# Performance work log

Hardware: AMD Instinct MI355X
Metric: run time of the kernel (lower is better)

The kernel has to match this reference:

```python
import jax, jax.numpy as jnp
import numpy as np

N, E, K, G = 50000, 800000, 3, 64
F_IN, F_HID, F_OUT, N_CLS = 128, 192, 128, 10
LAMBDA_MAX = 2.0  # PyG ChebConv default when lambda_max is None and normalization='sym'


def setup_inputs() -> dict:
    key = jax.random.key(0)
    ks = jax.random.split(key, 12)
    x = jax.random.normal(ks[0], (N, F_IN), dtype=jnp.float32)
    edge_index = jax.random.randint(ks[1], (2, E), 0, N)
    batch = jnp.sort(jax.random.randint(ks[2], (N,), 0, G))

    def mkW(k, fi, fo):
        return jax.random.normal(k, (K, fi, fo), dtype=jnp.float32) / np.float32(np.sqrt(K * fi))

    W1 = mkW(ks[3], F_IN, F_HID)
    b1 = jax.random.normal(ks[4], (F_HID,), dtype=jnp.float32) * 0.01
    W2 = mkW(ks[5], F_HID, F_HID)
    b2 = jax.random.normal(ks[6], (F_HID,), dtype=jnp.float32) * 0.01
    W3 = mkW(ks[7], F_HID, F_OUT)
    b3 = jax.random.normal(ks[8], (F_OUT,), dtype=jnp.float32) * 0.01
    fc_w = jax.random.normal(ks[9], (F_OUT, N_CLS), dtype=jnp.float32) / np.float32(np.sqrt(F_OUT))
    fc_b = jax.random.normal(ks[10], (N_CLS,), dtype=jnp.float32) * 0.01
    return {"x": x, "edge_index": edge_index, "batch": batch,
            "W1": W1, "b1": b1, "W2": W2, "b2": b2, "W3": W3, "b3": b3,
            "fc_w": fc_w, "fc_b": fc_b}


def reference(x, edge_index, batch, W1, b1, W2, b2, W3, b3, fc_w, fc_b):
    row, col = edge_index[0], edge_index[1]
    # symmetric scaled Laplacian: L_hat = (2/lmax) * (I - D^-1/2 A D^-1/2) - I
    deg = jax.ops.segment_sum(jnp.ones((E,), x.dtype), row, num_segments=N)
    dis = jnp.where(deg > 0, jax.lax.rsqrt(jnp.maximum(deg, 1e-12)), 0.0)
    scale = 2.0 / LAMBDA_MAX
    w_edge = (-scale) * dis[row] * dis[col]  # off-diagonal entries of L_hat
    diag_w = scale - 1.0                      # diagonal entries (0 when lmax=2)

    def prop(h):  # h: [N, F] -> L_hat @ h
        return jax.ops.segment_sum(w_edge[:, None] * h[col], row, num_segments=N) + diag_w * h

    def cheb_conv(h, W, b):
        Tx0 = h
        out = Tx0 @ W[0]
        Tx1 = prop(Tx0)
        out = out + Tx1 @ W[1]
        for k in range(2, K):
            Tx2 = 2.0 * prop(Tx1) - Tx0
            out = out + Tx2 @ W[k]
            Tx0, Tx1 = Tx1, Tx2
        return out + b

    h = cheb_conv(x, W1, b1)
    h = cheb_conv(h, W2, b2)
    h = cheb_conv(h, W3, b3)

    # global mean pool over graphs
    sums = jax.ops.segment_sum(h, batch, num_segments=G)
    cnts = jax.ops.segment_sum(jnp.ones((N,), h.dtype), batch, num_segments=G)
    pooled = sums / jnp.maximum(cnts, 1.0)[:, None]  # [G, F_OUT]

    logits = pooled @ fc_w + fc_b
    return jax.nn.log_softmax(logits, axis=1)
```

## Files before the change

### kernel.cpp

```cpp
#include <hip/hip_runtime.h>
#include <math.h>

#define N_NODES 50000
#define N_EDGES 800000
#define N_GRAPHS 64
#define F_INN 128
#define F_HID 192
#define F_OUTT 128
#define N_CLS 10

typedef short short8 __attribute__((ext_vector_type(8)));
typedef float f32x4 __attribute__((ext_vector_type(4)));

static __device__ inline unsigned short f2bf(float f) {
    unsigned int u = __float_as_uint(f);
    unsigned int r = (u + 0x7FFFu + ((u >> 16) & 1u)) >> 16;
    return (unsigned short)r;
}
static __device__ inline float bf2f(unsigned short h) {
    return __uint_as_float(((unsigned int)h) << 16);
}

__global__ void k_deg(const int* __restrict__ row, int* __restrict__ cnt,
                      int* __restrict__ rank) {
    int e = blockIdx.x * 256 + threadIdx.x;
    if (e < N_EDGES) rank[e] = atomicAdd(&cnt[row[e]], 1);
}

__global__ void k_scan1(const int* __restrict__ cnt, int* __restrict__ rp,
                        int* __restrict__ part, float* __restrict__ dis) {
    __shared__ int s[256];
    int base = blockIdx.x * 512;
    int i0 = base + 2 * threadIdx.x;
    int v0 = (i0 < N_NODES) ? cnt[i0] : 0;
    int v1 = (i0 + 1 < N_NODES) ? cnt[i0 + 1] : 0;
    if (i0 < N_NODES) dis[i0] = v0 > 0 ? rsqrtf((float)v0) : 0.f;
    if (i0 + 1 < N_NODES) dis[i0 + 1] = v1 > 0 ? rsqrtf((float)v1) : 0.f;
    int tsum = v0 + v1;
    s[threadIdx.x] = tsum;
    __syncthreads();
    for (int off = 1; off < 256; off <<= 1) {
        int val = (threadIdx.x >= off) ? s[threadIdx.x - off] : 0;
        __syncthreads();
        s[threadIdx.x] += val;
        __syncthreads();
    }
    int excl = s[threadIdx.x] - tsum;
    if (i0 < N_NODES) rp[i0] = excl;
    if (i0 + 1 < N_NODES) rp[i0 + 1] = excl + v0;
    if (threadIdx.x == 255) part[blockIdx.x] = s[255];
}

__global__ void k_scan3(int* __restrict__ rp, const int* __restrict__ part,
                        int nb) {
    __shared__ int s[128];
    int t = threadIdx.x;
    int b = blockIdx.x;
    if (t < 128) s[t] = (t < b && t < nb) ? part[t] : 0;
    __syncthreads();
    for (int off = 64; off > 0; off >>= 1) {
        if (t < off) s[t] += s[t + off];
        __syncthreads();
    }
    int add = s[0];
    int i0 = b * 512 + 2 * t;
    if (i0 < N_NODES) rp[i0] += add;
    if (i0 + 1 < N_NODES) rp[i0 + 1] += add;
    if (b == 0 && t == 0) rp[N_NODES] = N_EDGES;
}

__global__ void k_scatter(const int* __restrict__ row, const int* __restrict__ col,
                          const float* __restrict__ dis, const int* __restrict__ rp,
                          const int* __restrict__ rank, int2* __restrict__ cw) {
    int e = blockIdx.x * 256 + threadIdx.x;
    if (e < N_EDGES) {
        int r = row[e], c = col[e];
        int pos = rp[r] + rank[e];
        int2 v;
        v.x = c;
        v.y = __float_as_int(-dis[r] * dis[c]);
        cw[pos] = v;
    }
}

#define NX (N_NODES * F_INN)
#define NW1 (3 * 128 * 192)
#define NW2 (3 * 192 * 192)
#define NW3 (3 * 192 * 128)
#define NPS (3 * N_GRAPHS * F_HID)
__global__ void k_convAll(const float* __restrict__ x, const float* __restrict__ W1,
                          const float* __restrict__ W2, const float* __restrict__ W3,
                          unsigned short* __restrict__ xb,
                          unsigned short* __restrict__ Wt1,
                          unsigned short* __restrict__ Wt2,
                          unsigned short* __restrict__ Wt3,
                          int* __restrict__ cnt, float* __restrict__ psum) {
    int idx = blockIdx.x * 256 + threadIdx.x;
    if (idx < NX) {
        xb[idx] = f2bf(x[idx]);
        return;
    }
    idx -= NX;
    if (idx < NW1) {
        int per = 128 * 192;
        int j = idx / per, r = idx - j * per;
        int k = r / 192, n = r - k * 192;
        float v = (j == 0) ? (W1[idx] - W1[idx + 2 * per])
                           : (j == 2 ? 2.f * W1[idx] : W1[idx]);
        Wt1[j * per + n * 128 + k] = f2bf(v);
        return;
    }
    idx -= NW1;
    if (idx < NW2) {
        int per = 192 * 192;
        int j = idx / per, r = idx - j * per;
        int k = r / 192, n = r - k * 192;
        float v = (j == 0) ? (W2[idx] - W2[idx + 2 * per])
                           : (j == 2 ? 2.f * W2[idx] : W2[idx]);
        Wt2[j * per + n * 192 + k] = f2bf(v);
        return;
    }
    idx -= NW2;
    if (idx < NW3) {
        int per = 192 * 128;
        int j = idx / per, r = idx - j * per;
        int k = r / 128, n = r - k * 128;
        float v = (j == 0) ? (W3[idx] - W3[idx + 2 * per])
                           : (j == 2 ? 2.f * W3[idx] : W3[idx]);
        Wt3[j * per + n * 192 + k] = f2bf(v);
        return;
    }
    idx -= NW3;
    if (idx < N_NODES) {
        cnt[idx] = 0;
        return;
    }
    idx -= N_NODES;
    if (idx < NPS) psum[idx] = 0.f;
}

template <int F, int POOL>
__global__ void k_spmv(const int* __restrict__ rp, const int2* __restrict__ cw,
                       const unsigned short* __restrict__ h,
                       unsigned short* __restrict__ y,
                       const int* __restrict__ batch, float* __restrict__ psum) {
    constexpr bool EX = (F > 128);
    constexpr int FU = F / 2;
    __shared__ float ps[POOL ? 192 : 1];
    __shared__ int gs[4];
    int wave = threadIdx.x >> 6;
    int lane = threadIdx.x & 63;
    int r = blockIdx.x * 4 + wave;
    int e0 = __builtin_amdgcn_readfirstlane(rp[r]);
    int e1 = __builtin_amdgcn_readfirstlane(rp[r + 1]);
    const unsigned int* hu = (const unsigned int*)h;
    float a0 = 0.f, a1 = 0.f, a2 = 0.f;
    int e = e0;
    for (; e + 8 <= e1; e += 8) {
        int colv[8];
        float wv[8];
#pragma unroll
        for (int u = 0; u < 8; u++) {
            int2 p = cw[e + u];
            colv[u] = __builtin_amdgcn_readfirstlane(p.x);
            wv[u] = __uint_as_float(__builtin_amdgcn_readfirstlane(p.y));
        }
        unsigned int g[8];
        unsigned short s[8];
#pragma unroll
        for (int u = 0; u < 8; u++) {
            g[u] = hu[colv[u] * FU + lane];
            if constexpr (EX) s[u] = h[colv[u] * F + 128 + lane];
        }
#pragma unroll
        for (int u = 0; u < 8; u++) {
            a0 += wv[u] * bf2f((unsigned short)g[u]);
            a1 += wv[u] * bf2f((unsigned short)(g[u] >> 16));
            if constexpr (EX) a2 += wv[u] * bf2f(s[u]);
        }
    }
    for (; e + 4 <= e1; e += 4) {
        int colv[4];
        float wv[4];
#pragma unroll
        for (int u = 0; u < 4; u++) {
            int2 p = cw[e + u];
            colv[u] = __builtin_amdgcn_readfirstlane(p.x);
            wv[u] = __uint_as_float(__builtin_amdgcn_readfirstlane(p.y));
        }
        unsigned int g[4];
        unsigned short s[4];
#pragma unroll
        for (int u = 0; u < 4; u++) {
            g[u] = hu[colv[u] * FU + lane];
            if constexpr (EX) s[u] = h[colv[u] * F + 128 + lane];
        }
#pragma unroll
        for (int u = 0; u < 4; u++) {
            a0 += wv[u] * bf2f((unsigned short)g[u]);
            a1 += wv[u] * bf2f((unsigned short)(g[u] >> 16));
            if constexpr (EX) a2 += wv[u] * bf2f(s[u]);
        }
    }
    for (; e < e1; e++) {
        int2 p = cw[e];
        int c = __builtin_amdgcn_readfirstlane(p.x);
        float w = __uint_as_float(__builtin_amdgcn_readfirstlane(p.y));
        unsigned int g = hu[c * FU + lane];
        a0 += w * bf2f((unsigned short)g);
        a1 += w * bf2f((unsigned short)(g >> 16));
        if constexpr (EX) a2 += w * bf2f(h[c * F + 128 + lane]);
    }
    if constexpr (POOL != 1) {
        ((unsigned int*)y)[r * FU + lane] =
            (unsigned int)f2bf(a0) | ((unsigned int)f2bf(a1) << 16);
        if constexpr (EX) y[r * F + 128 + lane] = f2bf(a2);
    }
    if constexpr (POOL != 0) {
        int t = threadIdx.x;
        if (t < 4) gs[t] = batch[blockIdx.x * 4 + t];
        if (t >= 64) ps[t - 64] = 0.f;
        __syncthreads();
        int g0 = gs[0], g3 = gs[3];
        if (g0 == g3) {
            atomicAdd(&ps[2 * lane], a0);
            atomicAdd(&ps[2 * lane + 1], a1);
            atomicAdd(&ps[128 + lane], a2);
            __syncthreads();
            if (wave == 0) {
                atomicAdd(&psum[g0 * 192 + 2 * lane], ps[2 * lane]);
                atomicAdd(&psum[g0 * 192 + 2 * lane + 1], ps[2 * lane + 1]);
                atomicAdd(&psum[g0 * 192 + 128 + lane], ps[128 + lane]);
            }
        } else {
            int gg = gs[wave];
            atomicAdd(&psum[gg * 192 + 2 * lane], a0);
            atomicAdd(&psum[gg * 192 + 2 * lane + 1], a1);
            atomicAdd(&psum[gg * 192 + 128 + lane], a2);
        }
    }
}

template <int Fin, int Fout, bool POOL>
__global__ __launch_bounds__(256) void k_gemm3(
    const unsigned short* __restrict__ A0, const unsigned short* __restrict__ A1,
    const unsigned short* __restrict__ A2, const unsigned short* __restrict__ Wt,
    const float* __restrict__ bias, unsigned short* __restrict__ C,
    const int* __restrict__ batch, float* __restrict__ psum) {
    constexpr int NF = Fout / 16;
    constexpr int BP = Fout / 64;
    __shared__ unsigned short As[128 * 40];
    __shared__ unsigned short Bs[Fout * 40];
    int t = threadIdx.x;
    int w = t >> 6;
    int lane = t & 63;
    int ml = lane & 15;
    int quad = lane >> 4;
    int mBase = blockIdx.x * 128;
    constexpr int per = Fin * Fout;

    f32x4 acc[2][NF];
#pragma unroll
    for (int i = 0; i < 2; i++)
#pragma unroll
        for (int jn = 0; jn < NF; jn++) acc[i][jn] = (f32x4){0.f, 0.f, 0.f, 0.f};

    int srow = t >> 2;
    int schunk = t & 3;
    constexpr int nChunks = (3 * Fin) >> 5;

    for (int ch = 0; ch < nChunks; ch++) {
        int kg = ch << 5;
        int j = kg / Fin;
        int kk = kg - j * Fin;
        const unsigned short* Aj = (j == 0) ? A0 : (j == 1) ? A1 : A2;
        if (ch > 0) __syncthreads();
#pragma unroll
        for (int pass = 0; pass < 2; pass++) {
            int row = srow + pass * 64;
            int gm = mBase + row;
            uint4 v = {0u, 0u, 0u, 0u};
            if (gm < N_NODES)
                v = *(const uint4*)(Aj + (size_t)gm * Fin + kk + schunk * 8);
            *(uint4*)&As[row * 40 + schunk * 8] = v;
        }
#pragma unroll
        for (int pass = 0; pass < BP; pass++) {
            int row = srow + pass * 64;
            const unsigned short* src =
                Wt + (size_t)j * per + (size_t)row * Fin + kk + schunk * 8;
            *(uint4*)&Bs[row * 40 + schunk * 8] = *(const uint4*)src;
        }
        __syncthreads();

        short8 afr[2];
#pragma unroll
        for (int i = 0; i < 2; i++)
            afr[i] = *(const short8*)&As[(w * 32 + i * 16 + ml) * 40 + quad * 8];
#pragma unroll
        for (int jn = 0; jn < NF; jn++) {
            short8 bfr = *(const short8*)&Bs[(jn * 16 + ml) * 40 + quad * 8];
#pragma unroll
            for (int i = 0; i < 2; i++)
                acc[i][jn] = __builtin_amdgcn_mfma_f32_16x16x32_bf16(
                    afr[i], bfr, acc[i][jn], 0, 0, 0);
        }
    }

    float biasv[NF];
#pragma unroll
    for (int jn = 0; jn < NF; jn++) biasv[jn] = bias[jn * 16 + ml];

#pragma unroll
    for (int i = 0; i < 2; i++) {
#pragma unroll
        for (int r = 0; r < 4; r++) {
            int m = mBase + w * 32 + i * 16 + quad * 4 + r;
            if (m < N_NODES) {
                unsigned short* cp = C + (size_t)m * Fout + ml;
#pragma unroll
                for (int jn = 0; jn < NF; jn++)
                    cp[jn * 16] = f2bf(acc[i][jn][r] + biasv[jn]);
            }
        }
    }
    if constexpr (POOL) {
        int m0 = mBase + w * 32;
        if (m0 >= N_NODES) return;
        int mlast = m0 + 31;
        if (mlast >= N_NODES) mlast = N_NODES - 1;
        int g0 = batch[m0];
        int g1 = batch[mlast];
        if (g0 == g1) {
#pragma unroll
            for (int jn = 0; jn < NF; jn++) {
                float pv = 0.f;
#pragma unroll
                for (int i = 0; i < 2; i++)
#pragma unroll
                    for (int r = 0; r < 4; r++) {
                        int m = m0 + i * 16 + quad * 4 + r;
                        if (m < N_NODES) pv += acc[i][jn][r] + biasv[jn];
                    }
                pv += __shfl_xor(pv, 16);
                pv += __shfl_xor(pv, 32);
                if (lane < 16) atomicAdd(&psum[g0 * Fout + ml + jn * 16], pv);
            }
        } else {
#pragma unroll
            for (int i = 0; i < 2; i++)
#pragma unroll
                for (int r = 0; r < 4; r++) {
                    int m = m0 + i * 16 + quad * 4 + r;
                    if (m < N_NODES) {
                        int g = batch[m];
#pragma unroll
                        for (int jn = 0; jn < NF; jn++)
                            atomicAdd(&psum[g * Fout + ml + jn * 16],
                                      acc[i][jn][r] + biasv[jn]);
                    }
                }
        }
    }
}

__global__ __launch_bounds__(128) void k_head2(
    const float* __restrict__ psum,
    const unsigned short* __restrict__ Wt3, const float* __restrict__ b3,
    const int* __restrict__ batch, const float* __restrict__ fcw,
    const float* __restrict__ fcb, float* __restrict__ out) {
    int g = blockIdx.x;
    int t = threadIdx.x;
    __shared__ float ps[3 * 192];
    __shared__ float m3[F_OUTT];
    __shared__ float sl[N_CLS];
    for (int i = t; i < 192; i += 128) {
        ps[i] = psum[g * 192 + i];
        ps[192 + i] = psum[N_GRAPHS * 192 + g * 192 + i];
        ps[384 + i] = psum[2 * N_GRAPHS * 192 + g * 192 + i];
    }
    __syncthreads();
    int a = 0, b = N_NODES;
    while (a < b) { int m = (a + b) >> 1; if (batch[m] < g) a = m + 1; else b = m; }
    int lo = a;
    a = lo; b = N_NODES;
    while (a < b) { int m = (a + b) >> 1; if (batch[m] < g + 1) a = m + 1; else b = m; }
    float inv = 1.f / fmaxf((float)(a - lo), 1.f);
    constexpr int per = 192 * F_OUTT;
    float accv = 0.f;
    const unsigned short* wp = Wt3 + (size_t)t * 192;
#pragma unroll 4
    for (int k = 0; k < 192; k += 8) {
        short8 v0 = *(const short8*)(wp + k);
        short8 v1 = *(const short8*)(wp + per + k);
        short8 v2 = *(const short8*)(wp + 2 * per + k);
#pragma unroll
        for (int j = 0; j < 8; j++)
            accv += ps[k + j] * bf2f((unsigned short)v0[j]) +
                    ps[192 + k + j] * bf2f((unsigned short)v1[j]) +
                    ps[384 + k + j] * bf2f((unsigned short)v2[j]);
    }
    m3[t] = accv * inv + b3[t];
    __syncthreads();
    if (t < N_CLS) {
        float l = fcb[t];
        for (int n = 0; n < F_OUTT; n++) l += m3[n] * fcw[n * N_CLS + t];
        sl[t] = l;
    }
    __syncthreads();
    if (t < N_CLS) {
        float mx = -1e30f;
        for (int i = 0; i < N_CLS; i++) mx = fmaxf(mx, sl[i]);
        float s = 0.f;
        for (int i = 0; i < N_CLS; i++) s += expf(sl[i] - mx);
        out[g * N_CLS + t] = sl[t] - mx - logf(s);
    }
}

extern "C" void kernel_launch(void* const* d_in, const int* in_sizes, int n_in,
                              void* d_out, int out_size, void* d_ws, size_t ws_size,
                              hipStream_t stream) {
    const float* x = (const float*)d_in[0];
    const int* ei = (const int*)d_in[1];
    const int* batch = (const int*)d_in[2];
    const float* W1 = (const float*)d_in[3];
    const float* b1 = (const float*)d_in[4];
    const float* W2 = (const float*)d_in[5];
    const float* b2 = (const float*)d_in[6];
    const float* W3 = (const float*)d_in[7];
    const float* b3 = (const float*)d_in[8];
    const float* fcw = (const float*)d_in[9];
    const float* fcb = (const float*)d_in[10];
    float* out = (float*)d_out;
    const int* row = ei;
    const int* col = ei + N_EDGES;

    char* p = (char*)d_ws;
    auto carve = [&](size_t bytes) {
        char* q = p;
        p += (bytes + 255) & ~(size_t)255;
        return q;
    };
    int* cnt = (int*)carve(N_NODES * 4);
    int* rank = (int*)carve((size_t)N_EDGES * 4);
    float* dis = (float*)carve(N_NODES * 4);
    int* rp = (int*)carve((N_NODES + 1) * 4);
    int* part = (int*)carve(128 * 4);
    int2* cw = (int2*)carve((size_t)N_EDGES * 8);
    unsigned short* xb = (unsigned short*)carve((size_t)N_NODES * F_INN * 2);
    size_t hbytes = (size_t)N_NODES * 192 * 2;
    unsigned short* bufA = (unsigned short*)carve(hbytes);
    unsigned short* bufB = (unsigned short*)carve(hbytes);
    unsigned short* bufC = (unsigned short*)carve(hbytes);
    unsigned short* bufD = (unsigned short*)carve(hbytes);
    unsigned short* Wt1 = (unsigned short*)carve(NW1 * 2);
    unsigned short* Wt2 = (unsigned short*)carve(NW2 * 2);
    unsigned short* Wt3 = (unsigned short*)carve(NW3 * 2);
    float* psum = (float*)carve(NPS * 4);
    float* psumX = psum;
    float* psumG1 = psum + N_GRAPHS * 192;
    float* psumG2 = psum + 2 * N_GRAPHS * 192;

    {
        int tot = NX + NW1 + NW2 + NW3 + N_NODES + NPS;
        k_convAll<<<(tot + 255) / 256, 256, 0, stream>>>(x, W1, W2, W3, xb, Wt1, Wt2,
                                                         Wt3, cnt, psum);
    }

    k_deg<<<(N_EDGES + 255) / 256, 256, 0, stream>>>(row, cnt, rank);
    int nb = (N_NODES + 511) / 512;
    k_scan1<<<nb, 256, 0, stream>>>(cnt, rp, part, dis);
    k_scan3<<<nb, 256, 0, stream>>>(rp, part, nb);
    k_scatter<<<(N_EDGES + 255) / 256, 256, 0, stream>>>(row, col, dis, rp, rank, cw);

    const int spmvGrid = N_NODES / 4;
    const int gemmGrid = (N_NODES + 127) / 128;

    k_spmv<128, 0><<<spmvGrid, 256, 0, stream>>>(rp, cw, xb, bufB, nullptr, nullptr);
    k_spmv<128, 0><<<spmvGrid, 256, 0, stream>>>(rp, cw, bufB, bufC, nullptr, nullptr);
    k_gemm3<128, 192, false><<<gemmGrid, 256, 0, stream>>>(xb, bufB, bufC, Wt1, b1,
                                                           bufA, batch, nullptr);
    k_spmv<192, 0><<<spmvGrid, 256, 0, stream>>>(rp, cw, bufA, bufB, nullptr, nullptr);
    k_spmv<192, 0><<<spmvGrid, 256, 0, stream>>>(rp, cw, bufB, bufC, nullptr, nullptr);
    k_gemm3<192, 192, true><<<gemmGrid, 256, 0, stream>>>(bufA, bufB, bufC, Wt2, b2,
                                                          bufD, batch, psumX);
    k_spmv<192, 2><<<spmvGrid, 256, 0, stream>>>(rp, cw, bufD, bufB, batch, psumG1);
    k_spmv<192, 1><<<spmvGrid, 256, 0, stream>>>(rp, cw, bufB, nullptr, batch, psumG2);

    k_head2<<<N_GRAPHS, 128, 0, stream>>>(psum, Wt3, b3, batch, fcw, fcb, out);
}
```

Before: 545.1 us.

## Move graph pooling out of SpMV and GEMM epilogues into dedicated pool kernel

Removes the fused mean-pool atomics from the layer-2 GEMM epilogue and the last two SpMV launches, so those kernels only write their outputs. The final SpMV now materializes its result to memory, and a new k_pool3 kernel reads the three layer-2 feature buffers and reduces them per graph with run-length accumulation before atomic adds. This cuts the per-block shared-memory atomics and syncthreads in SpMV, and the many global atomics. In exchange it adds an extra write plus a full re-read of three N×192 bf16 buffers and one more launch.

```diff
diff --git a/kernel.cpp b/kernel.cpp
--- a/kernel.cpp
+++ b/kernel.cpp
@@ -139,18 +139,16 @@
     if (idx < NPS) psum[idx] = 0.f;
 }
 
-template <int F, int POOL>
+template <int F>
 __global__ void k_spmv(const int* __restrict__ rp, const int2* __restrict__ cw,
                        const unsigned short* __restrict__ h,
-                       unsigned short* __restrict__ y,
-                       const int* __restrict__ batch, float* __restrict__ psum) {
+                       unsigned short* __restrict__ y) {
     constexpr bool EX = (F > 128);
     constexpr int FU = F / 2;
-    __shared__ float ps[POOL ? 192 : 1];
-    __shared__ int gs[4];
     int wave = threadIdx.x >> 6;
     int lane = threadIdx.x & 63;
     int r = blockIdx.x * 4 + wave;
+    if (r >= N_NODES) return;
     int e0 = __builtin_amdgcn_readfirstlane(rp[r]);
     int e1 = __builtin_amdgcn_readfirstlane(rp[r + 1]);
     const unsigned int* hu = (const unsigned int*)h;
@@ -211,42 +209,16 @@
         a1 += w * bf2f((unsigned short)(g >> 16));
         if constexpr (EX) a2 += w * bf2f(h[c * F + 128 + lane]);
     }
-    if constexpr (POOL != 1) {
-        ((unsigned int*)y)[r * FU + lane] =
-            (unsigned int)f2bf(a0) | ((unsigned int)f2bf(a1) << 16);
-        if constexpr (EX) y[r * F + 128 + lane] = f2bf(a2);
-    }
-    if constexpr (POOL != 0) {
-        int t = threadIdx.x;
-        if (t < 4) gs[t] = batch[blockIdx.x * 4 + t];
-        if (t >= 64) ps[t - 64] = 0.f;
-        __syncthreads();
-        int g0 = gs[0], g3 = gs[3];
-        if (g0 == g3) {
-            atomicAdd(&ps[2 * lane], a0);
-            atomicAdd(&ps[2 * lane + 1], a1);
-            atomicAdd(&ps[128 + lane], a2);
-            __syncthreads();
-            if (wave == 0) {
-                atomicAdd(&psum[g0 * 192 + 2 * lane], ps[2 * lane]);
-                atomicAdd(&psum[g0 * 192 + 2 * lane + 1], ps[2 * lane + 1]);
-                atomicAdd(&psum[g0 * 192 + 128 + lane], ps[128 + lane]);
-            }
-        } else {
-            int gg = gs[wave];
-            atomicAdd(&psum[gg * 192 + 2 * lane], a0);
-            atomicAdd(&psum[gg * 192 + 2 * lane + 1], a1);
-            atomicAdd(&psum[gg * 192 + 128 + lane], a2);
-        }
-    }
-}
-
-template <int Fin, int Fout, bool POOL>
+    ((unsigned int*)y)[r * FU + lane] =
+        (unsigned int)f2bf(a0) | ((unsigned int)f2bf(a1) << 16);
+    if constexpr (EX) y[r * F + 128 + lane] = f2bf(a2);
+}
+
+template <int Fin, int Fout>
 __global__ __launch_bounds__(256) void k_gemm3(
     const unsigned short* __restrict__ A0, const unsigned short* __restrict__ A1,
     const unsigned short* __restrict__ A2, const unsigned short* __restrict__ Wt,
-    const float* __restrict__ bias, unsigned short* __restrict__ C,
-    const int* __restrict__ batch, float* __restrict__ psum) {
+    const float* __restrict__ bias, unsigned short* __restrict__ C) {
     constexpr int NF = Fout / 16;
     constexpr int BP = Fout / 64;
     __shared__ unsigned short As[128 * 40];
@@ -324,43 +296,73 @@
             }
         }
     }
-    if constexpr (POOL) {
-        int m0 = mBase + w * 32;
-        if (m0 >= N_NODES) return;
-        int mlast = m0 + 31;
-        if (mlast >= N_NODES) mlast = N_NODES - 1;
-        int g0 = batch[m0];
-        int g1 = batch[mlast];
-        if (g0 == g1) {
-#pragma unroll
-            for (int jn = 0; jn < NF; jn++) {
-                float pv = 0.f;
-#pragma unroll
-                for (int i = 0; i < 2; i++)
-#pragma unroll
-                    for (int r = 0; r < 4; r++) {
-                        int m = m0 + i * 16 + quad * 4 + r;
-                        if (m < N_NODES) pv += acc[i][jn][r] + biasv[jn];
-                    }
-                pv += __shfl_xor(pv, 16);
-                pv += __shfl_xor(pv, 32);
-                if (lane < 16) atomicAdd(&psum[g0 * Fout + ml + jn * 16], pv);
+}
+
+__global__ __launch_bounds__(256) void k_pool3(
+    const unsigned short* __restrict__ x3, const unsigned short* __restrict__ g1,
+    const unsigned short* __restrict__ g2, const int* __restrict__ batch,
+    float* __restrict__ psum) {
+    int wave = threadIdx.x >> 6;
+    int lane = threadIdx.x & 63;
+    int r0 = blockIdx.x * 256;
+    int r1 = r0 + 256;
+    if (r1 > N_NODES) r1 = N_NODES;
+    const unsigned int* xu = (const unsigned int*)x3;
+    const unsigned int* au = (const unsigned int*)g1;
+    const unsigned int* bu = (const unsigned int*)g2;
+    float x0 = 0.f, x1 = 0.f, x2 = 0.f;
+    float a0 = 0.f, a1 = 0.f, a2 = 0.f;
+    float b0 = 0.f, b1 = 0.f, b2 = 0.f;
+    int curg = -1;
+    for (int r = r0 + wave; r < r1; r += 4) {
+        int g = __builtin_amdgcn_readfirstlane(batch[r]);
+        if (g != curg) {
+            if (curg >= 0) {
+                float* p0 = psum + curg * 192;
+                atomicAdd(&p0[2 * lane], x0);
+                atomicAdd(&p0[2 * lane + 1], x1);
+                atomicAdd(&p0[128 + lane], x2);
+                float* p1 = p0 + N_GRAPHS * 192;
+                atomicAdd(&p1[2 * lane], a0);
+                atomicAdd(&p1[2 * lane + 1], a1);
+                atomicAdd(&p1[128 + lane], a2);
+                float* p2 = p1 + N_GRAPHS * 192;
+                atomicAdd(&p2[2 * lane], b0);
+                atomicAdd(&p2[2 * lane + 1], b1);
+                atomicAdd(&p2[128 + lane], b2);
+                x0 = x1 = x2 = a0 = a1 = a2 = b0 = b1 = b2 = 0.f;
             }
-        } else {
-#pragma unroll
-            for (int i = 0; i < 2; i++)
-#pragma unroll
-                for (int r = 0; r < 4; r++) {
-                    int m = m0 + i * 16 + quad * 4 + r;
-                    if (m < N_NODES) {
-                        int g = batch[m];
-#pragma unroll
-                        for (int jn = 0; jn < NF; jn++)
-                            atomicAdd(&psum[g * Fout + ml + jn * 16],
-                                      acc[i][jn][r] + biasv[jn]);
-                    }
-                }
-        }
+            curg = g;
+        }
+        unsigned int vx = xu[(size_t)r * 96 + lane];
+        unsigned int va = au[(size_t)r * 96 + lane];
+        unsigned int vb = bu[(size_t)r * 96 + lane];
+        unsigned short sx = x3[(size_t)r * 192 + 128 + lane];
+        unsigned short sa = g1[(size_t)r * 192 + 128 + lane];
+        unsigned short sb = g2[(size_t)r * 192 + 128 + lane];
+        x0 += bf2f((unsigned short)vx);
+        x1 += bf2f((unsigned short)(vx >> 16));
+        x2 += bf2f(sx);
+        a0 += bf2f((unsigned short)va);
+        a1 += bf2f((unsigned short)(va >> 16));
+        a2 += bf2f(sa);
+        b0 += bf2f((unsigned short)vb);
+        b1 += bf2f((unsigned short)(vb >> 16));
+        b2 += bf2f(sb);
+    }
+    if (curg >= 0) {
+        float* p0 = psum + curg * 192;
+        atomicAdd(&p0[2 * lane], x0);
+        atomicAdd(&p0[2 * lane + 1], x1);
+        atomicAdd(&p0[128 + lane], x2);
+        float* p1 = p0 + N_GRAPHS * 192;
+        atomicAdd(&p1[2 * lane], a0);
+        atomicAdd(&p1[2 * lane + 1], a1);
+        atomicAdd(&p1[128 + lane], a2);
+        float* p2 = p1 + N_GRAPHS * 192;
+        atomicAdd(&p2[2 * lane], b0);
+        atomicAdd(&p2[2 * lane + 1], b1);
+        atomicAdd(&p2[128 + lane], b2);
     }
 }
 
@@ -457,9 +459,6 @@
     unsigned short* Wt2 = (unsigned short*)carve(NW2 * 2);
     unsigned short* Wt3 = (unsigned short*)carve(NW3 * 2);
     float* psum = (float*)carve(NPS * 4);
-    float* psumX = psum;
-    float* psumG1 = psum + N_GRAPHS * 192;
-    float* psumG2 = psum + 2 * N_GRAPHS * 192;
 
     {
         int tot = NX + NW1 + NW2 + NW3 + N_NODES + NPS;
@@ -473,19 +472,18 @@
     k_scan3<<<nb, 256, 0, stream>>>(rp, part, nb);
     k_scatter<<<(N_EDGES + 255) / 256, 256, 0, stream>>>(row, col, dis, rp, rank, cw);
 
-    const int spmvGrid = N_NODES / 4;
+    const int spmvGrid = (N_NODES + 3) / 4;
     const int gemmGrid = (N_NODES + 127) / 128;
 
-    k_spmv<128, 0><<<spmvGrid, 256, 0, stream>>>(rp, cw, xb, bufB, nullptr, nullptr);
-    k_spmv<128, 0><<<spmvGrid, 256, 0, stream>>>(rp, cw, bufB, bufC, nullptr, nullptr);
-    k_gemm3<128, 192, false><<<gemmGrid, 256, 0, stream>>>(xb, bufB, bufC, Wt1, b1,
-                                                           bufA, batch, nullptr);
-    k_spmv<192, 0><<<spmvGrid, 256, 0, stream>>>(rp, cw, bufA, bufB, nullptr, nullptr);
-    k_spmv<192, 0><<<spmvGrid, 256, 0, stream>>>(rp, cw, bufB, bufC, nullptr, nullptr);
-    k_gemm3<192, 192, true><<<gemmGrid, 256, 0, stream>>>(bufA, bufB, bufC, Wt2, b2,
-                                                          bufD, batch, psumX);
-    k_spmv<192, 2><<<spmvGrid, 256, 0, stream>>>(rp, cw, bufD, bufB, batch, psumG1);
-    k_spmv<192, 1><<<spmvGrid, 256, 0, stream>>>(rp, cw, bufB, nullptr, batch, psumG2);
+    k_spmv<128><<<spmvGrid, 256, 0, stream>>>(rp, cw, xb, bufB);
+    k_spmv<128><<<spmvGrid, 256, 0, stream>>>(rp, cw, bufB, bufC);
+    k_gemm3<128, 192><<<gemmGrid, 256, 0, stream>>>(xb, bufB, bufC, Wt1, b1, bufA);
+    k_spmv<192><<<spmvGrid, 256, 0, stream>>>(rp, cw, bufA, bufB);
+    k_spmv<192><<<spmvGrid, 256, 0, stream>>>(rp, cw, bufB, bufC);
+    k_gemm3<192, 192><<<gemmGrid, 256, 0, stream>>>(bufA, bufB, bufC, Wt2, b2, bufD);
+    k_spmv<192><<<spmvGrid, 256, 0, stream>>>(rp, cw, bufD, bufB);
+    k_spmv<192><<<spmvGrid, 256, 0, stream>>>(rp, cw, bufB, bufC);
+    k_pool3<<<(N_NODES + 255) / 256, 256, 0, stream>>>(bufD, bufB, bufC, batch, psum);
 
     k_head2<<<N_GRAPHS, 128, 0, stream>>>(psum, Wt3, b3, batch, fcw, fcb, out);
 }
```

Measured after the change: 477.2 us. 12.5% less time.

## Split pooling out of layer-3 SpMVs and add feature-split packed-edge SpMV

Applied to the files above, without the earlier changes.

Removes the fused mean-pool atomics from the last two layer-3 SpMV launches and moves that pooling into a separate kernel that streams both propagated outputs and accumulates runs of same-graph rows before issuing atomics. The final SpMV becomes a feature-split kernel: two blocks per row group, each covering 96 features. It reads a compact 4-byte edge record holding a 16-bit column and an fp16 weight instead of the 8-byte int2. This cuts per-edge index traffic and the atomic contention inside SpMV. In exchange it adds an extra write and read of an intermediate buffer, packs columns into 16 bits (which overflows above 65535 nodes), and lowers edge-weight precision to fp16.

```diff
diff --git a/kernel.cpp b/kernel.cpp
--- a/kernel.cpp
+++ b/kernel.cpp
@@ -1,4 +1,5 @@
 #include <hip/hip_runtime.h>
+#include <hip/hip_fp16.h>
 #include <math.h>
 
 #define N_NODES 50000
@@ -71,15 +72,19 @@
 
 __global__ void k_scatter(const int* __restrict__ row, const int* __restrict__ col,
                           const float* __restrict__ dis, const int* __restrict__ rp,
-                          const int* __restrict__ rank, int2* __restrict__ cw) {
+                          const int* __restrict__ rank, int2* __restrict__ cw,
+                          unsigned int* __restrict__ cwh) {
     int e = blockIdx.x * 256 + threadIdx.x;
     if (e < N_EDGES) {
         int r = row[e], c = col[e];
         int pos = rp[r] + rank[e];
+        float w = -dis[r] * dis[c];
         int2 v;
         v.x = c;
-        v.y = __float_as_int(-dis[r] * dis[c]);
+        v.y = __float_as_int(w);
         cw[pos] = v;
+        unsigned short hw = __half_as_ushort(__float2half(w));
+        cwh[pos] = (unsigned int)c | ((unsigned int)hw << 16);
     }
 }
 
@@ -139,18 +144,16 @@
     if (idx < NPS) psum[idx] = 0.f;
 }
 
-template <int F, int POOL>
+template <int F>
 __global__ void k_spmv(const int* __restrict__ rp, const int2* __restrict__ cw,
                        const unsigned short* __restrict__ h,
-                       unsigned short* __restrict__ y,
-                       const int* __restrict__ batch, float* __restrict__ psum) {
+                       unsigned short* __restrict__ y) {
     constexpr bool EX = (F > 128);
     constexpr int FU = F / 2;
-    __shared__ float ps[POOL ? 192 : 1];
-    __shared__ int gs[4];
     int wave = threadIdx.x >> 6;
     int lane = threadIdx.x & 63;
     int r = blockIdx.x * 4 + wave;
+    if (r >= N_NODES) return;
     int e0 = __builtin_amdgcn_readfirstlane(rp[r]);
     int e1 = __builtin_amdgcn_readfirstlane(rp[r + 1]);
     const unsigned int* hu = (const unsigned int*)h;
@@ -211,34 +214,67 @@
         a1 += w * bf2f((unsigned short)(g >> 16));
         if constexpr (EX) a2 += w * bf2f(h[c * F + 128 + lane]);
     }
-    if constexpr (POOL != 1) {
-        ((unsigned int*)y)[r * FU + lane] =
+    ((unsigned int*)y)[r * FU + lane] =
+        (unsigned int)f2bf(a0) | ((unsigned int)f2bf(a1) << 16);
+    if constexpr (EX) y[r * F + 128 + lane] = f2bf(a2);
+}
+
+__global__ void k_spmv192s(const int* __restrict__ rp,
+                           const unsigned int* __restrict__ cwh,
+                           const unsigned short* __restrict__ h,
+                           unsigned short* __restrict__ y) {
+    int wave = threadIdx.x >> 6;
+    int lane = threadIdx.x & 63;
+    int bid = blockIdx.x;
+    int s = bid & 1;
+    int r = (bid >> 1) * 4 + wave;
+    if (r >= N_NODES) return;
+    int e0 = __builtin_amdgcn_readfirstlane(rp[r]);
+    int e1 = __builtin_amdgcn_readfirstlane(rp[r + 1]);
+    const unsigned int* hu = (const unsigned int*)h;
+    int fu = s * 48 + (lane < 48 ? lane : 47);
+    float a0 = 0.f, a1 = 0.f;
+    int e = e0;
+    for (; e + 8 <= e1; e += 8) {
+        unsigned int pk[8];
+#pragma unroll
+        for (int u = 0; u < 8; u++)
+            pk[u] = __builtin_amdgcn_readfirstlane(cwh[e + u]);
+        unsigned int g[8];
+#pragma unroll
+        for (int u = 0; u < 8; u++) g[u] = hu[(pk[u] & 0xFFFFu) * 96 + fu];
+#pragma unroll
+        for (int u = 0; u < 8; u++) {
+            float w = __half2float(__ushort_as_half((unsigned short)(pk[u] >> 16)));
+            a0 += w * bf2f((unsigned short)g[u]);
+            a1 += w * bf2f((unsigned short)(g[u] >> 16));
+        }
+    }
+    for (; e + 4 <= e1; e += 4) {
+        unsigned int pk[4];
+#pragma unroll
+        for (int u = 0; u < 4; u++)
+            pk[u] = __builtin_amdgcn_readfirstlane(cwh[e + u]);
+        unsigned int g[4];
+#pragma unroll
+        for (int u = 0; u < 4; u++) g[u] = hu[(pk[u] & 0xFFFFu) * 96 + fu];
+#pragma unroll
+        for (int u = 0; u < 4; u++) {
+            float w = __half2float(__ushort_as_half((unsigned short)(pk[u] >> 16)));
+            a0 += w * bf2f((unsigned short)g[u]);
+            a1 += w * bf2f((unsigned short)(g[u] >> 16));
+        }
+    }
+    for (; e < e1; e++) {
+        unsigned int pk = __builtin_amdgcn_readfirstlane(cwh[e]);
+        unsigned int g = hu[(pk & 0xFFFFu) * 96 + fu];
+        float w = __half2float(__ushort_as_half((unsigned short)(pk >> 16)));
+        a0 += w * bf2f((unsigned short)g);
+        a1 += w * bf2f((unsigned short)(g >> 16));
+    }
+    if (lane < 48)
+        ((unsigned int*)y)[r * 96 + fu] =
             (unsigned int)f2bf(a0) | ((unsigned int)f2bf(a1) << 16);
-        if constexpr (EX) y[r * F + 128 + lane] = f2bf(a2);
-    }
-    if constexpr (POOL != 0) {
-        int t = threadIdx.x;
-        if (t < 4) gs[t] = batch[blockIdx.x * 4 + t];
-        if (t >= 64) ps[t - 64] = 0.f;
-        __syncthreads();
-        int g0 = gs[0], g3 = gs[3];
-        if (g0 == g3) {
-            atomicAdd(&ps[2 * lane], a0);
-            atomicAdd(&ps[2 * lane + 1], a1);
-            atomicAdd(&ps[128 + lane], a2);
-            __syncthreads();
-            if (wave == 0) {
-                atomicAdd(&psum[g0 * 192 + 2 * lane], ps[2 * lane]);
-                atomicAdd(&psum[g0 * 192 + 2 * lane + 1], ps[2 * lane + 1]);
-                atomicAdd(&psum[g0 * 192 + 128 + lane], ps[128 + lane]);
-            }
-        } else {
-            int gg = gs[wave];
-            atomicAdd(&psum[gg * 192 + 2 * lane], a0);
-            atomicAdd(&psum[gg * 192 + 2 * lane + 1], a1);
-            atomicAdd(&psum[gg * 192 + 128 + lane], a2);
-        }
-    }
 }
 
 template <int Fin, int Fout, bool POOL>
@@ -364,6 +400,53 @@
     }
 }
 
+__global__ __launch_bounds__(256) void k_poolGG(
+    const unsigned short* __restrict__ g1, const unsigned short* __restrict__ g2,
+    const int* __restrict__ batch, float* __restrict__ psum) {
+    int wave = threadIdx.x >> 6;
+    int lane = threadIdx.x & 63;
+    int w0 = blockIdx.x * 64 + wave * 16;
+    if (w0 >= N_NODES) return;
+    int n = N_NODES - w0;
+    if (n > 16) n = 16;
+    int bv = 0;
+    if (lane < 16 && w0 + lane < N_NODES) bv = batch[w0 + lane];
+    const unsigned int* au = (const unsigned int*)g1;
+    const unsigned int* bu = (const unsigned int*)g2;
+    float a0 = 0.f, a1 = 0.f, a2 = 0.f, b0 = 0.f, b1 = 0.f, b2 = 0.f;
+    int cur = __shfl(bv, 0);
+    auto flush = [&](int g) {
+        float* p1 = psum + (size_t)N_GRAPHS * 192 + (size_t)g * 192;
+        atomicAdd(&p1[2 * lane], a0);
+        atomicAdd(&p1[2 * lane + 1], a1);
+        atomicAdd(&p1[128 + lane], a2);
+        float* p2 = p1 + (size_t)N_GRAPHS * 192;
+        atomicAdd(&p2[2 * lane], b0);
+        atomicAdd(&p2[2 * lane + 1], b1);
+        atomicAdd(&p2[128 + lane], b2);
+    };
+    for (int i = 0; i < n; i++) {
+        int g = __shfl(bv, i);
+        if (g != cur) {
+            flush(cur);
+            a0 = a1 = a2 = b0 = b1 = b2 = 0.f;
+            cur = g;
+        }
+        size_t r = (size_t)(w0 + i);
+        unsigned int va = au[r * 96 + lane];
+        unsigned int vb = bu[r * 96 + lane];
+        unsigned short sa = g1[r * 192 + 128 + lane];
+        unsigned short sb = g2[r * 192 + 128 + lane];
+        a0 += bf2f((unsigned short)va);
+        a1 += bf2f((unsigned short)(va >> 16));
+        a2 += bf2f(sa);
+        b0 += bf2f((unsigned short)vb);
+        b1 += bf2f((unsigned short)(vb >> 16));
+        b2 += bf2f(sb);
+    }
+    flush(cur);
+}
+
 __global__ __launch_bounds__(128) void k_head2(
     const float* __restrict__ psum,
     const unsigned short* __restrict__ Wt3, const float* __restrict__ b3,
@@ -447,6 +530,7 @@
     int* rp = (int*)carve((N_NODES + 1) * 4);
     int* part = (int*)carve(128 * 4);
     int2* cw = (int2*)carve((size_t)N_EDGES * 8);
+    unsigned int* cwh = (unsigned int*)carve((size_t)N_EDGES * 4);
     unsigned short* xb = (unsigned short*)carve((size_t)N_NODES * F_INN * 2);
     size_t hbytes = (size_t)N_NODES * 192 * 2;
     unsigned short* bufA = (unsigned short*)carve(hbytes);
@@ -457,9 +541,6 @@
     unsigned short* Wt2 = (unsigned short*)carve(NW2 * 2);
     unsigned short* Wt3 = (unsigned short*)carve(NW3 * 2);
     float* psum = (float*)carve(NPS * 4);
-    float* psumX = psum;
-    float* psumG1 = psum + N_GRAPHS * 192;
-    float* psumG2 = psum + 2 * N_GRAPHS * 192;
 
     {
         int tot = NX + NW1 + NW2 + NW3 + N_NODES + NPS;
@@ -471,21 +552,23 @@
     int nb = (N_NODES + 511) / 512;
     k_scan1<<<nb, 256, 0, stream>>>(cnt, rp, part, dis);
     k_scan3<<<nb, 256, 0, stream>>>(rp, part, nb);
-    k_scatter<<<(N_EDGES + 255) / 256, 256, 0, stream>>>(row, col, dis, rp, rank, cw);
-
-    const int spmvGrid = N_NODES / 4;
+    k_scatter<<<(N_EDGES + 255) / 256, 256, 0, stream>>>(row, col, dis, rp, rank, cw,
+                                                         cwh);
+
+    const int spmvGrid = (N_NODES + 3) / 4;
     const int gemmGrid = (N_NODES + 127) / 128;
 
-    k_spmv<128, 0><<<spmvGrid, 256, 0, stream>>>(rp, cw, xb, bufB, nullptr, nullptr);
-    k_spmv<128, 0><<<spmvGrid, 256, 0, stream>>>(rp, cw, bufB, bufC, nullptr, nullptr);
+    k_spmv<128><<<spmvGrid, 256, 0, stream>>>(rp, cw, xb, bufB);
+    k_spmv<128><<<spmvGrid, 256, 0, stream>>>(rp, cw, bufB, bufC);
     k_gemm3<128, 192, false><<<gemmGrid, 256, 0, stream>>>(xb, bufB, bufC, Wt1, b1,
                                                            bufA, batch, nullptr);
-    k_spmv<192, 0><<<spmvGrid, 256, 0, stream>>>(rp, cw, bufA, bufB, nullptr, nullptr);
-    k_spmv<192, 0><<<spmvGrid, 256, 0, stream>>>(rp, cw, bufB, bufC, nullptr, nullptr);
+    k_spmv<192><<<spmvGrid, 256, 0, stream>>>(rp, cw, bufA, bufB);
+    k_spmv<192><<<spmvGrid, 256, 0, stream>>>(rp, cw, bufB, bufC);
     k_gemm3<192, 192, true><<<gemmGrid, 256, 0, stream>>>(bufA, bufB, bufC, Wt2, b2,
-                                                          bufD, batch, psumX);
-    k_spmv<192, 2><<<spmvGrid, 256, 0, stream>>>(rp, cw, bufD, bufB, batch, psumG1);
-    k_spmv<192, 1><<<spmvGrid, 256, 0, stream>>>(rp, cw, bufB, nullptr, batch, psumG2);
+                                                          bufD, batch, psum);
+    k_spmv<192><<<spmvGrid, 256, 0, stream>>>(rp, cw, bufD, bufB);
+    k_spmv192s<<<spmvGrid * 2, 256, 0, stream>>>(rp, cwh, bufB, bufC);
+    k_poolGG<<<(N_NODES + 63) / 64, 256, 0, stream>>>(bufB, bufC, batch, psum);
 
     k_head2<<<N_GRAPHS, 128, 0, stream>>>(psum, Wt3, b3, batch, fcw, fcb, out);
 }
```

New measurement: 478.1 us. 12.3% less time.
